# Performance work log

Measured on AMD Instinct MI355X. Metric: run time of the kernel, lower is better.

The kernel has to match this reference:

```python
import jax, jax.numpy as jnp
import numpy as np

N_NODES = 100000
N_EDGES = 1600000
D_IN = 64
D_OUT = 64
NUM_ETYPE = 2
NEG_SLOPE = 0.2


def setup_inputs() -> dict:
    key = jax.random.key(0)
    ks = jax.random.split(key, 9)
    feat = jax.random.normal(ks[0], (N_NODES, D_IN), dtype=jnp.float32)
    rel = jax.random.uniform(ks[1], (N_EDGES, NUM_ETYPE), dtype=jnp.float32)
    W_self = jax.random.normal(ks[2], (D_OUT, D_IN), dtype=jnp.float32) * 0.1
    b_self = jax.random.normal(ks[3], (D_OUT,), dtype=jnp.float32) * 0.1
    W_neigh = jax.random.normal(ks[4], (D_OUT, D_IN), dtype=jnp.float32) * 0.1
    b_neigh = jax.random.normal(ks[5], (D_OUT,), dtype=jnp.float32) * 0.1
    attn_e = jax.random.normal(ks[6], (NUM_ETYPE, 1), dtype=jnp.float32)
    src = jax.random.randint(ks[7], (N_EDGES,), 0, N_NODES, dtype=jnp.int32)
    dst = jax.random.randint(ks[8], (N_EDGES,), 0, N_NODES, dtype=jnp.int32)
    return {"feat": feat, "rel": rel, "W_self": W_self, "b_self": b_self,
            "W_neigh": W_neigh, "b_neigh": b_neigh, "attn_e": attn_e,
            "src": src, "dst": dst}


def reference(feat, rel, W_self, b_self, W_neigh, b_neigh, attn_e, src, dst):
    n = feat.shape[0]
    # per-edge attention score: [E, num_etype] @ [num_etype, 1] -> [E]
    e = jnp.squeeze(rel @ attn_e, axis=1)
    e = jax.nn.leaky_relu(e, negative_slope=NEG_SLOPE)
    # edge_softmax: segment softmax over edges grouped by destination node
    emax = jax.ops.segment_max(e, dst, num_segments=n)          # [N]
    ex = jnp.exp(e - emax[dst])                                  # [E]
    denom = jax.ops.segment_sum(ex, dst, num_segments=n)        # [N]
    a = ex / denom[dst]                                          # [E]
    # u_mul_e + sum aggregation: neigh[v] = sum_e a_e * feat[src_e]
    m = feat[src] * a[:, None]                                   # [E, D_IN]
    h_neigh = jax.ops.segment_sum(m, dst, num_segments=n)       # [N, D_IN]
    # rst = fc_self(h_self) + fc_neigh(h_neigh)  (torch Linear: x @ W.T + b)
    return feat @ W_self.T + b_self + h_neigh @ W_neigh.T + b_neigh
```

## Files before the change

### kernel.cpp

```cpp
#include <hip/hip_runtime.h>
#include <hip/hip_bf16.h>

#define N_NODES 100000
#define N_EDGES 1600000
#define D 64
#define NEG_SLOPE 0.2f

#define BSHIFT 10
#define BNODES 1024
#define NBUCK ((N_NODES + BNODES - 1) >> BSHIFT)
#define BUCKET_CAP 17408
#define P1_EPB 4096
#define P1_T 512
#define P1_IT (P1_EPB / P1_T)

__global__ __launch_bounds__(P1_T) void binning_kernel(
    const float2* __restrict__ rel, const float* __restrict__ attn_e,
    const int* __restrict__ src, const int* __restrict__ dst,
    int* __restrict__ bucket_cursor, uint2* __restrict__ binned)
{
    __shared__ uint2 staged1[P1_EPB];
    __shared__ uint2 staged2[P1_EPB];
    __shared__ int cnt[NBUCK];
    __shared__ int excl[NBUCK];
    __shared__ int chunkbase[NBUCK];

    int tid = threadIdx.x;
    int e0 = blockIdx.x * P1_EPB;
    int n = min(P1_EPB, N_EDGES - e0);

    for (int b = tid; b < NBUCK; b += P1_T) cnt[b] = 0;
    __syncthreads();

    float a0 = attn_e[0], a1 = attn_e[1];

    int myslot[P1_IT];
    #pragma unroll
    for (int j = 0; j < P1_IT; ++j) {
        int i = tid + j * P1_T;
        if (i < n) {
            int e = e0 + i;
            float2 r = rel[e];
            float sc = r.x * a0 + r.y * a1;
            sc = (sc > 0.f) ? sc : NEG_SLOPE * sc;
            float ev = __expf(sc);
            unsigned u = __float_as_uint(ev) + 0x8000u;
            unsigned wcode = (u >> 16) & 0x7FFFu;
            unsigned s = (unsigned)src[e];
            unsigned d = (unsigned)dst[e];
            staged1[i] = make_uint2((s << 15) | wcode, d);
            myslot[j] = atomicAdd(&cnt[d >> BSHIFT], 1);
        }
    }
    __syncthreads();
    if (tid == 0) {
        int run = 0;
        for (int b = 0; b < NBUCK; ++b) { excl[b] = run; run += cnt[b]; }
    }
    __syncthreads();
    #pragma unroll
    for (int j = 0; j < P1_IT; ++j) {
        int i = tid + j * P1_T;
        if (i < n) {
            uint2 v = staged1[i];
            staged2[excl[v.y >> BSHIFT] + myslot[j]] = v;
        }
    }
    if (tid < NBUCK)
        chunkbase[tid] = atomicAdd(&bucket_cursor[tid], cnt[tid]);
    __syncthreads();
    for (int i = tid; i < n; i += P1_T) {
        uint2 v = staged2[i];
        int b = (int)(v.y >> BSHIFT);
        binned[(size_t)b * BUCKET_CAP + chunkbase[b] + (i - excl[b])] = v;
    }
}

__global__ __launch_bounds__(1024) void csr_kernel(
    const int* __restrict__ bucket_cursor, const uint2* __restrict__ binned,
    int* __restrict__ offsets, unsigned* __restrict__ edata)
{
    __shared__ unsigned vals[BUCKET_CAP];
    __shared__ int hist[BNODES];
    __shared__ int nexcl[BNODES];
    __shared__ int cur[BNODES];
    __shared__ int bc[NBUCK];
    __shared__ int base_sh;

    int b = blockIdx.x;
    int tid = threadIdx.x;

    if (tid < NBUCK) bc[tid] = bucket_cursor[tid];
    hist[tid] = 0;
    cur[tid] = 0;
    __syncthreads();
    if (tid == 0) {
        int s = 0;
        for (int i = 0; i < b; ++i) s += bc[i];
        base_sh = s;
    }
    __syncthreads();
    int count = bc[b];
    int base = base_sh;
    const uint2* bin = binned + (size_t)b * BUCKET_CAP;

    for (int i = tid; i < count; i += 1024)
        atomicAdd(&hist[bin[i].y & (BNODES - 1)], 1);
    __syncthreads();

    int h = hist[tid];
    nexcl[tid] = h;
    __syncthreads();
    for (int d = 1; d < BNODES; d <<= 1) {
        int u = (tid >= d) ? nexcl[tid - d] : 0;
        __syncthreads();
        nexcl[tid] += u;
        __syncthreads();
    }
    int excl = nexcl[tid] - h;
    __syncthreads();
    nexcl[tid] = excl;
    __syncthreads();

    int node = (b << BSHIFT) + tid;
    if (node < N_NODES) offsets[node] = base + excl;
    if (b == NBUCK - 1 && tid == 0) offsets[N_NODES] = N_EDGES;

    for (int i = tid; i < count; i += 1024) {
        uint2 e = bin[i];
        int d = e.y & (BNODES - 1);
        int t = atomicAdd(&cur[d], 1);
        vals[nexcl[d] + t] = e.x;
    }
    __syncthreads();
    for (int i = tid; i < count; i += 1024)
        edata[base + i] = vals[i];
}

__global__ __launch_bounds__(512) void gemm_fused_kernel(
    const float* __restrict__ feat, const float* __restrict__ W_self,
    const float* __restrict__ W_neigh, const float* __restrict__ b_self,
    const float* __restrict__ b_neigh, float* __restrict__ out,
    __hip_bfloat16* __restrict__ g)
{
    __shared__ float Wt[2][D][D + 1];
    __shared__ float fs[64 * D];
    int tid = threadIdx.x;
    #pragma unroll
    for (int i = 0; i < 8; ++i) {
        int idx = tid + i * 512;
        Wt[0][idx & 63][idx >> 6] = W_self[idx];
        Wt[1][idx & 63][idx >> 6] = W_neigh[idx];
    }
    {
        long base4 = (long)blockIdx.x * 1024;
        const float4* f4 = (const float4*)feat;
        float4* s4 = (float4*)fs;
        #pragma unroll
        for (int i = 0; i < 2; ++i) {
            int idx = tid + i * 512;
            if (base4 + idx < (long)N_NODES * D / 4) s4[idx] = f4[base4 + idx];
        }
    }
    __syncthreads();

    int lane = tid & 63;
    int wave = tid >> 6;
    int m = wave >> 2;
    int sw = wave & 3;
    float w[D];
    #pragma unroll
    for (int k = 0; k < D; ++k) w[k] = Wt[m][k][lane];
    float bias = (m == 0) ? (b_self[lane] + b_neigh[lane]) : 0.f;

    int r0 = blockIdx.x * 64 + sw * 16;
    #pragma unroll 1
    for (int rr = 0; rr < 16; ++rr) {
        int r = r0 + rr;
        if (r >= N_NODES) break;
        const float4* frow = (const float4*)(fs + (sw * 16 + rr) * D);
        float acc = 0.f;
        #pragma unroll
        for (int k4 = 0; k4 < 16; ++k4) {
            float4 f = frow[k4];
            acc += f.x * w[4*k4]   + f.y * w[4*k4+1]
                 + f.z * w[4*k4+2] + f.w * w[4*k4+3];
        }
        if (m == 0) out[(size_t)r * D + lane] = acc + bias;
        else        g[(size_t)r * D + lane] = __float2bfloat16(acc);
    }
}

__global__ __launch_bounds__(256) void aggregate_kernel(
    const uint* __restrict__ g32, const unsigned* __restrict__ edata,
    const int* __restrict__ offsets, float* __restrict__ out)
{
    int v = blockIdx.x * 4 + (threadIdx.x >> 6);
    int lane = threadIdx.x & 63;
    int q = lane >> 4;
    int t = lane & 15;
    int lo = offsets[v], hi = offsets[v + 1];
    float4 acc = make_float4(0.f, 0.f, 0.f, 0.f);
    float sum = 0.f;

    for (int i = lo; i < hi; i += 8) {
        int e0 = i + q;
        int e1 = i + 4 + q;
        int ec0 = (e0 < hi) ? e0 : hi - 1;
        int ec1 = (e1 < hi) ? e1 : hi - 1;
        unsigned p0 = edata[ec0];
        unsigned p1 = edata[ec1];
        float w0 = (e0 < hi) ? __uint_as_float((p0 & 0x7FFFu) << 16) : 0.f;
        float w1 = (e1 < hi) ? __uint_as_float((p1 & 0x7FFFu) << 16) : 0.f;
        const uint2* r0 = (const uint2*)(g32 + (size_t)(p0 >> 15) * (D / 2));
        const uint2* r1 = (const uint2*)(g32 + (size_t)(p1 >> 15) * (D / 2));
        uint2 u0 = r0[t];
        uint2 u1 = r1[t];
        acc.x += w0 * __uint_as_float(u0.x << 16);
        acc.y += w0 * __uint_as_float(u0.x & 0xFFFF0000u);
        acc.z += w0 * __uint_as_float(u0.y << 16);
        acc.w += w0 * __uint_as_float(u0.y & 0xFFFF0000u);
        sum += w0;
        acc.x += w1 * __uint_as_float(u1.x << 16);
        acc.y += w1 * __uint_as_float(u1.x & 0xFFFF0000u);
        acc.z += w1 * __uint_as_float(u1.y << 16);
        acc.w += w1 * __uint_as_float(u1.y & 0xFFFF0000u);
        sum += w1;
    }
    #pragma unroll
    for (int mm = 16; mm <= 32; mm <<= 1) {
        acc.x += __shfl_xor(acc.x, mm, 64);
        acc.y += __shfl_xor(acc.y, mm, 64);
        acc.z += __shfl_xor(acc.z, mm, 64);
        acc.w += __shfl_xor(acc.w, mm, 64);
        sum   += __shfl_xor(sum,   mm, 64);
    }
    if (hi > lo && q == 0) {
        float inv = 1.f / sum;
        float4* orow = (float4*)(out + (size_t)v * D);
        float4 c = orow[t];
        c.x += acc.x * inv; c.y += acc.y * inv;
        c.z += acc.z * inv; c.w += acc.w * inv;
        orow[t] = c;
    }
}

extern "C" void kernel_launch(void* const* d_in, const int* in_sizes, int n_in,
                              void* d_out, int out_size, void* d_ws, size_t ws_size,
                              hipStream_t stream) {
    const float* feat    = (const float*)d_in[0];
    const float* rel     = (const float*)d_in[1];
    const float* W_self  = (const float*)d_in[2];
    const float* b_self  = (const float*)d_in[3];
    const float* W_neigh = (const float*)d_in[4];
    const float* b_neigh = (const float*)d_in[5];
    const float* attn_e  = (const float*)d_in[6];
    const int*   src     = (const int*)d_in[7];
    const int*   dst     = (const int*)d_in[8];
    float* out = (float*)d_out;

    uint2* binned = (uint2*)d_ws;
    __hip_bfloat16* g = (__hip_bfloat16*)(binned + (size_t)NBUCK * BUCKET_CAP);
    unsigned* edata = (unsigned*)((char*)g + (size_t)N_NODES * D * 2);
    int* offsets = (int*)(edata + N_EDGES);
    int* bucket_cursor = offsets + N_NODES + 1;

    hipMemsetAsync(bucket_cursor, 0, NBUCK * sizeof(int), stream);

    binning_kernel<<<(N_EDGES + P1_EPB - 1) / P1_EPB, P1_T, 0, stream>>>(
        (const float2*)rel, attn_e, src, dst, bucket_cursor, binned);
    csr_kernel<<<NBUCK, 1024, 0, stream>>>(
        bucket_cursor, binned, offsets, edata);
    gemm_fused_kernel<<<(N_NODES + 63) / 64, 512, 0, stream>>>(
        feat, W_self, W_neigh, b_self, b_neigh, out, g);
    aggregate_kernel<<<N_NODES / 4, 256, 0, stream>>>(
        (const uint*)g, edata, offsets, out);
}
```

Baseline: 215.1 us.

## Use split-bf16 MFMA for node GEMMs and unroll aggregation to 16 edges

Rewrites the self and neighbor linear projections to use 16x16x32 bf16 MFMA instructions. It emulates fp32 accuracy with a hi/lo bf16 split (three MFMAs per product), reading feat and weights directly from global memory instead of staging them in LDS. The launch now uses 128 rows per block. Separately, the aggregation loop processes 16 edges per iteration instead of 8 to expose more memory-level parallelism. This trades scalar FMA work for extra conversion ALU and more register pressure, and drops some accuracy relative to full fp32.

```diff
diff --git a/kernel.cpp b/kernel.cpp
--- a/kernel.cpp
+++ b/kernel.cpp
@@ -137,57 +137,80 @@
         edata[base + i] = vals[i];
 }
 
+typedef __attribute__((ext_vector_type(8))) short bf16x8;
+typedef __attribute__((ext_vector_type(4))) float f32x4;
+#define MFMA16(a, b, c) __builtin_amdgcn_mfma_f32_16x16x32_bf16(a, b, c, 0, 0, 0)
+
+__device__ __forceinline__ short bf16_rne(float f) {
+    unsigned u = __float_as_uint(f);
+    u += 0x7FFFu + ((u >> 16) & 1u);
+    return (short)(u >> 16);
+}
+__device__ __forceinline__ float bf16_to_f(short h) {
+    return __uint_as_float(((unsigned)(unsigned short)h) << 16);
+}
+__device__ __forceinline__ void cvt8(float4 f0, float4 f1,
+                                     bf16x8& hi, bf16x8& lo) {
+    float v[8] = {f0.x, f0.y, f0.z, f0.w, f1.x, f1.y, f1.z, f1.w};
+    #pragma unroll
+    for (int j = 0; j < 8; ++j) {
+        short h = bf16_rne(v[j]);
+        hi[j] = h;
+        lo[j] = bf16_rne(v[j] - bf16_to_f(h));
+    }
+}
+
 __global__ __launch_bounds__(512) void gemm_fused_kernel(
     const float* __restrict__ feat, const float* __restrict__ W_self,
     const float* __restrict__ W_neigh, const float* __restrict__ b_self,
     const float* __restrict__ b_neigh, float* __restrict__ out,
     __hip_bfloat16* __restrict__ g)
 {
-    __shared__ float Wt[2][D][D + 1];
-    __shared__ float fs[64 * D];
     int tid = threadIdx.x;
-    #pragma unroll
-    for (int i = 0; i < 8; ++i) {
-        int idx = tid + i * 512;
-        Wt[0][idx & 63][idx >> 6] = W_self[idx];
-        Wt[1][idx & 63][idx >> 6] = W_neigh[idx];
-    }
-    {
-        long base4 = (long)blockIdx.x * 1024;
-        const float4* f4 = (const float4*)feat;
-        float4* s4 = (float4*)fs;
-        #pragma unroll
-        for (int i = 0; i < 2; ++i) {
-            int idx = tid + i * 512;
-            if (base4 + idx < (long)N_NODES * D / 4) s4[idx] = f4[base4 + idx];
-        }
-    }
-    __syncthreads();
-
     int lane = tid & 63;
     int wave = tid >> 6;
-    int m = wave >> 2;
-    int sw = wave & 3;
-    float w[D];
-    #pragma unroll
-    for (int k = 0; k < D; ++k) w[k] = Wt[m][k][lane];
-    float bias = (m == 0) ? (b_self[lane] + b_neigh[lane]) : 0.f;
-
-    int r0 = blockIdx.x * 64 + sw * 16;
-    #pragma unroll 1
-    for (int rr = 0; rr < 16; ++rr) {
-        int r = r0 + rr;
-        if (r >= N_NODES) break;
-        const float4* frow = (const float4*)(fs + (sw * 16 + rr) * D);
-        float acc = 0.f;
+    int llo = lane & 15;
+    int lhi = lane >> 4;
+    int rb = blockIdx.x * 128 + wave * 16;
+    if (rb >= N_NODES) return;
+
+    int arow = rb + llo;
+    if (arow > N_NODES - 1) arow = N_NODES - 1;
+    const float4* fr = (const float4*)(feat + (size_t)arow * D);
+    bf16x8 ahi[2], alo[2];
+    #pragma unroll
+    for (int s = 0; s < 2; ++s)
+        cvt8(fr[s * 8 + lhi * 2], fr[s * 8 + lhi * 2 + 1], ahi[s], alo[s]);
+
+    unsigned short* g16 = (unsigned short*)g;
+    #pragma unroll
+    for (int nt = 0; nt < 4; ++nt) {
+        int col = nt * 16 + llo;
+        const float4* ws = (const float4*)(W_self + (size_t)col * D);
+        const float4* wn = (const float4*)(W_neigh + (size_t)col * D);
+        f32x4 accS = {0.f, 0.f, 0.f, 0.f};
+        f32x4 accN = {0.f, 0.f, 0.f, 0.f};
         #pragma unroll
-        for (int k4 = 0; k4 < 16; ++k4) {
-            float4 f = frow[k4];
-            acc += f.x * w[4*k4]   + f.y * w[4*k4+1]
-                 + f.z * w[4*k4+2] + f.w * w[4*k4+3];
+        for (int s = 0; s < 2; ++s) {
+            bf16x8 bh, bl;
+            cvt8(ws[s * 8 + lhi * 2], ws[s * 8 + lhi * 2 + 1], bh, bl);
+            accS = MFMA16(ahi[s], bh, accS);
+            accS = MFMA16(alo[s], bh, accS);
+            accS = MFMA16(ahi[s], bl, accS);
+            cvt8(wn[s * 8 + lhi * 2], wn[s * 8 + lhi * 2 + 1], bh, bl);
+            accN = MFMA16(ahi[s], bh, accN);
+            accN = MFMA16(alo[s], bh, accN);
+            accN = MFMA16(ahi[s], bl, accN);
         }
-        if (m == 0) out[(size_t)r * D + lane] = acc + bias;
-        else        g[(size_t)r * D + lane] = __float2bfloat16(acc);
+        float bias = b_self[col] + b_neigh[col];
+        #pragma unroll
+        for (int rg = 0; rg < 4; ++rg) {
+            int r = rb + lhi * 4 + rg;
+            if (r < N_NODES) {
+                out[(size_t)r * D + col] = accS[rg] + bias;
+                g16[(size_t)r * D + col] = (unsigned short)bf16_rne(accN[rg]);
+            }
+        }
     }
 }
 
@@ -203,19 +226,31 @@
     float4 acc = make_float4(0.f, 0.f, 0.f, 0.f);
     float sum = 0.f;
 
-    for (int i = lo; i < hi; i += 8) {
+    for (int i = lo; i < hi; i += 16) {
         int e0 = i + q;
         int e1 = i + 4 + q;
+        int e2 = i + 8 + q;
+        int e3 = i + 12 + q;
         int ec0 = (e0 < hi) ? e0 : hi - 1;
         int ec1 = (e1 < hi) ? e1 : hi - 1;
+        int ec2 = (e2 < hi) ? e2 : hi - 1;
+        int ec3 = (e3 < hi) ? e3 : hi - 1;
         unsigned p0 = edata[ec0];
         unsigned p1 = edata[ec1];
+        unsigned p2 = edata[ec2];
+        unsigned p3 = edata[ec3];
         float w0 = (e0 < hi) ? __uint_as_float((p0 & 0x7FFFu) << 16) : 0.f;
         float w1 = (e1 < hi) ? __uint_as_float((p1 & 0x7FFFu) << 16) : 0.f;
+        float w2 = (e2 < hi) ? __uint_as_float((p2 & 0x7FFFu) << 16) : 0.f;
+        float w3 = (e3 < hi) ? __uint_as_float((p3 & 0x7FFFu) << 16) : 0.f;
         const uint2* r0 = (const uint2*)(g32 + (size_t)(p0 >> 15) * (D / 2));
         const uint2* r1 = (const uint2*)(g32 + (size_t)(p1 >> 15) * (D / 2));
+        const uint2* r2 = (const uint2*)(g32 + (size_t)(p2 >> 15) * (D / 2));
+        const uint2* r3 = (const uint2*)(g32 + (size_t)(p3 >> 15) * (D / 2));
         uint2 u0 = r0[t];
         uint2 u1 = r1[t];
+        uint2 u2 = r2[t];
+        uint2 u3 = r3[t];
         acc.x += w0 * __uint_as_float(u0.x << 16);
         acc.y += w0 * __uint_as_float(u0.x & 0xFFFF0000u);
         acc.z += w0 * __uint_as_float(u0.y << 16);
@@ -226,6 +261,16 @@
         acc.z += w1 * __uint_as_float(u1.y << 16);
         acc.w += w1 * __uint_as_float(u1.y & 0xFFFF0000u);
         sum += w1;
+        acc.x += w2 * __uint_as_float(u2.x << 16);
+        acc.y += w2 * __uint_as_float(u2.x & 0xFFFF0000u);
+        acc.z += w2 * __uint_as_float(u2.y << 16);
+        acc.w += w2 * __uint_as_float(u2.y & 0xFFFF0000u);
+        sum += w2;
+        acc.x += w3 * __uint_as_float(u3.x << 16);
+        acc.y += w3 * __uint_as_float(u3.x & 0xFFFF0000u);
+        acc.z += w3 * __uint_as_float(u3.y << 16);
+        acc.w += w3 * __uint_as_float(u3.y & 0xFFFF0000u);
+        sum += w3;
     }
     #pragma unroll
     for (int mm = 16; mm <= 32; mm <<= 1) {
@@ -271,7 +316,7 @@
         (const float2*)rel, attn_e, src, dst, bucket_cursor, binned);
     csr_kernel<<<NBUCK, 1024, 0, stream>>>(
         bucket_cursor, binned, offsets, edata);
-    gemm_fused_kernel<<<(N_NODES + 63) / 64, 512, 0, stream>>>(
+    gemm_fused_kernel<<<(N_NODES + 127) / 128, 512, 0, stream>>>(
         feat, W_self, W_neigh, b_self, b_neigh, out, g);
     aggregate_kernel<<<N_NODES / 4, 256, 0, stream>>>(
         (const uint*)g, edata, offsets, out);
```

Measured after the change: 206.8 us. 1.04x faster.
